# Kernel optimization log

Measured on AMD Instinct MI355X. Metric: run time of the kernel, lower is better.

Reference implementation:

```python
import jax, jax.numpy as jnp
import numpy as np

H = 64  # hidden_dim


def _lstm_layer(x, w_ih, w_hh, b_ih, b_hh):
    # x: [B,T,I]; w_ih: [4H,I]; w_hh: [4H,H]; gate order (PyTorch): i,f,g,o
    B = x.shape[0]
    xp = jnp.einsum('bti,gi->btg', x, w_ih) + b_ih + b_hh  # [B,T,4H]
    h0 = jnp.zeros((B, H), x.dtype)
    c0 = jnp.zeros((B, H), x.dtype)

    def step(carry, xt):
        h, c = carry
        g = xt + h @ w_hh.T  # [B,4H]
        i, f, gg, o = jnp.split(g, 4, axis=-1)
        c = jax.nn.sigmoid(f) * c + jax.nn.sigmoid(i) * jnp.tanh(gg)
        h = jax.nn.sigmoid(o) * jnp.tanh(c)
        return (h, c), h

    _, ys = jax.lax.scan(step, (h0, c0), xp.transpose(1, 0, 2))  # [T,B,H]
    return ys.transpose(1, 0, 2)


def _gru_layer(x, w_ih, w_hh, b_ih, b_hh):
    # x: [B,T,I]; w_ih: [3H,I]; w_hh: [3H,H]; gate order (PyTorch): r,z,n
    B = x.shape[0]
    xp = jnp.einsum('bti,gi->btg', x, w_ih) + b_ih  # [B,T,3H]
    h0 = jnp.zeros((B, H), x.dtype)

    def step(h, xt):
        hp = h @ w_hh.T + b_hh  # [B,3H]
        xr, xz, xn = jnp.split(xt, 3, axis=-1)
        hr, hz, hn = jnp.split(hp, 3, axis=-1)
        r = jax.nn.sigmoid(xr + hr)
        z = jax.nn.sigmoid(xz + hz)
        n = jnp.tanh(xn + r * hn)
        h = (1.0 - z) * n + z * h
        return h, h

    _, ys = jax.lax.scan(step, h0, xp.transpose(1, 0, 2))
    return ys.transpose(1, 0, 2)


def setup_inputs() -> dict:
    key = jax.random.key(0)
    ks = jax.random.split(key, 20)
    s = 1.0 / np.sqrt(H)  # PyTorch default uniform(-1/sqrt(H), 1/sqrt(H))
    u = lambda k, shp: jax.random.uniform(k, shp, jnp.float32, -s, s)
    B, T, I = 2048, 512, 1
    return {
        'x': jax.random.normal(ks[0], (B, T, I), jnp.float32),
        # LSTM layer 0 (input I) and layer 1 (input H)
        'lw_ih0': u(ks[1], (4 * H, I)), 'lw_hh0': u(ks[2], (4 * H, H)),
        'lb_ih0': u(ks[3], (4 * H,)), 'lb_hh0': u(ks[4], (4 * H,)),
        'lw_ih1': u(ks[5], (4 * H, H)), 'lw_hh1': u(ks[6], (4 * H, H)),
        'lb_ih1': u(ks[7], (4 * H,)), 'lb_hh1': u(ks[8], (4 * H,)),
        # GRU layer 0 and 1 (input H)
        'gw_ih0': u(ks[9], (3 * H, H)), 'gw_hh0': u(ks[10], (3 * H, H)),
        'gb_ih0': u(ks[11], (3 * H,)), 'gb_hh0': u(ks[12], (3 * H,)),
        'gw_ih1': u(ks[13], (3 * H, H)), 'gw_hh1': u(ks[14], (3 * H, H)),
        'gb_ih1': u(ks[15], (3 * H,)), 'gb_hh1': u(ks[16], (3 * H,)),
        # fc head
        'fc_w': u(ks[17], (1, H)), 'fc_b': u(ks[18], (1,)),
    }


def reference(x, lw_ih0, lw_hh0, lb_ih0, lb_hh0, lw_ih1, lw_hh1, lb_ih1, lb_hh1,
              gw_ih0, gw_hh0, gb_ih0, gb_hh0, gw_ih1, gw_hh1, gb_ih1, gb_hh1,
              fc_w, fc_b):
    out = _lstm_layer(x, lw_ih0, lw_hh0, lb_ih0, lb_hh0)
    out = _lstm_layer(out, lw_ih1, lw_hh1, lb_ih1, lb_hh1)
    out = _gru_layer(out, gw_ih0, gw_hh0, gb_ih0, gb_hh0)
    out = _gru_layer(out, gw_ih1, gw_hh1, gb_ih1, gb_hh1)
    return out[:, -1, :] @ fc_w.T + fc_b  # [B,1]
```

## Files before the change

### kernel.cpp

```cpp
#include <hip/hip_runtime.h>


#define TT 512
#define SR 72
#define SLOT (16 * SR)
#define LOG2E 1.44269504f

typedef __attribute__((ext_vector_type(8))) short bfrag;
typedef __attribute__((ext_vector_type(4))) float facc;

#define MFMA(a,b,c) __builtin_amdgcn_mfma_f32_16x16x32_bf16((a),(b),(c),0,0,0)

__device__ __forceinline__ float sigmP(float u){
  return __builtin_amdgcn_rcpf(1.0f + __builtin_amdgcn_exp2f(u));
}
__device__ __forceinline__ float tanhP(float u){
  return 2.0f * __builtin_amdgcn_rcpf(1.0f + __builtin_amdgcn_exp2f(u)) - 1.0f;
}
__device__ __forceinline__ void spin_ge(volatile int* p, int tgt){
  while (*p < tgt) {}
}
__device__ __forceinline__ facc bcast4(float v){
  facc b; b[0] = v; b[1] = v; b[2] = v; b[3] = v; return b;
}
__device__ __forceinline__ short f2bf(float f){
  union { float f; unsigned u; } v; v.f = f;
  return (short)((v.u + 0x7fffu + ((v.u >> 16) & 1u)) >> 16);
}
__device__ __forceinline__ unsigned pk_bf16(float lo, float hi){
  unsigned r;
  asm("v_cvt_pk_bf16_f32 %0, %1, %2" : "=v"(r) : "v"(lo), "v"(hi));
  return r;
}

__global__ __launch_bounds__(1024) void rnn_fused(
    const float* __restrict__ x,
    const float* __restrict__ lw_ih0, const float* __restrict__ lw_hh0,
    const float* __restrict__ lb_ih0, const float* __restrict__ lb_hh0,
    const float* __restrict__ lw_ih1, const float* __restrict__ lw_hh1,
    const float* __restrict__ lb_ih1, const float* __restrict__ lb_hh1,
    const float* __restrict__ gw_ih0, const float* __restrict__ gw_hh0,
    const float* __restrict__ gb_ih0, const float* __restrict__ gb_hh0,
    const float* __restrict__ gw_ih1, const float* __restrict__ gw_hh1,
    const float* __restrict__ gb_ih1, const float* __restrict__ gb_hh1,
    const float* __restrict__ fc_w, const float* __restrict__ fc_b,
    float* __restrict__ out)
{
  __shared__ __align__(16) short S0[4 * SLOT];
  __shared__ __align__(16) short S1[4 * SLOT];
  __shared__ __align__(16) short S2[4 * SLOT];
  __shared__ __align__(16) short S3[4 * SLOT];
  __shared__ float xs[8][TT];
  __shared__ float hfin[8][68];
  __shared__ int cnt[4];

  const int tid = threadIdx.x;
  const int w     = tid >> 6;
  const int layer = w >> 2;
  const int lo4   = w & 3;
  const int l   = tid & 63;
  const int lq  = l >> 4;
  const int lc  = l & 15;
  const int kb  = lq * 8;
  const int rb0 = blockIdx.x * 8;
  const int wrbase = (4 * lq) * SR + lo4 * 16 + lc;
  volatile int* vc = cnt;

  const float SS  = -LOG2E;
  const float ST2 = -2.0f * LOG2E;

  {
    const int idx = tid * 4;
    const int row = idx >> 9, t0 = idx & 511;
    *(float4*)&xs[row][t0] = *(const float4*)(x + (rb0 + row) * TT + t0);
  }
  for (int i = tid; i < 4 * SLOT; i += 1024) {
    S0[i] = 0; S1[i] = 0; S2[i] = 0; S3[i] = 0;
  }
  if (tid < 4) cnt[tid] = 0;
  __syncthreads();

  if (layer == 0) {
    bfrag wf[4][2];
    float wxs[4];
    facc b4[4];
    #pragma unroll
    for (int G = 0; G < 4; ++G) {
      const float sc = (G == 2) ? ST2 : SS;
      const int col = G * 64 + lo4 * 16 + lc;
      #pragma unroll
      for (int kt = 0; kt < 2; ++kt) {
        bfrag f;
        #pragma unroll
        for (int j = 0; j < 8; ++j)
          f[j] = f2bf(sc * lw_hh0[col * 64 + kt * 32 + kb + j]);
        wf[G][kt] = f;
      }
      wxs[G] = sc * lw_ih0[col];
      b4[G]  = bcast4(sc * (lb_ih0[col] + lb_hh0[col]));
    }
    float c0[2] = {0.f, 0.f};
    for (int tb = 0; tb < TT / 4; ++tb) {
      const float4 xv0 = *(const float4*)&xs[2 * lq][tb * 4];
      const float4 xv1 = *(const float4*)&xs[2 * lq + 1][tb * 4];
      const float* xp0 = (const float*)&xv0;
      const float* xp1 = (const float*)&xv1;
      #pragma unroll
      for (int u = 0; u < 4; ++u) {
        const int t = tb * 4 + u;
        if (tb >= 1) spin_ge(vc + 1, 4 * (t - 3));
        if (tb > 0 || u > 0) spin_ge(vc + 0, 4 * t);
        __threadfence_block();
        const short* s = S0 + ((u + 3) & 3) * SLOT;
        const bfrag a0 = *(const bfrag*)(s + lc * SR + kb);
        const bfrag a1 = *(const bfrag*)(s + lc * SR + 32 + kb);
        facc acc[4];
        #pragma unroll
        for (int G = 0; G < 4; ++G) {
          facc z = MFMA(a0, wf[G][0], b4[G]);
          z = MFMA(a1, wf[G][1], z);
          acc[G] = z;
        }
        float hh[2];
        #pragma unroll
        for (int m = 0; m < 2; ++m) {
          const float xv = m ? xp1[u] : xp0[u];
          const float i_ = sigmP(acc[0][m] + xv * wxs[0]);
          const float f_ = sigmP(acc[1][m] + xv * wxs[1]);
          const float g_ = tanhP(acc[2][m] + xv * wxs[2]);
          const float o_ = sigmP(acc[3][m] + xv * wxs[3]);
          c0[m] = f_ * c0[m] + i_ * g_;
          hh[m] = o_ * tanhP(c0[m] * ST2);
        }
        const unsigned pk = pk_bf16(hh[0], hh[1]);
        short* d = S0 + u * SLOT;
        d[wrbase]      = (short)pk;
        d[wrbase + SR] = (short)(pk >> 16);
        __threadfence_block();
        if (l == 0) atomicAdd(&cnt[0], 1);
      }
    }
  } else if (layer == 1) {
    bfrag wxf[4][2], whf[4][2];
    facc b4[4];
    #pragma unroll
    for (int G = 0; G < 4; ++G) {
      const float sc = (G == 2) ? ST2 : SS;
      const int col = G * 64 + lo4 * 16 + lc;
      #pragma unroll
      for (int kt = 0; kt < 2; ++kt) {
        bfrag f0, f1;
        #pragma unroll
        for (int j = 0; j < 8; ++j) {
          const int o = col * 64 + kt * 32 + kb + j;
          f0[j] = f2bf(sc * lw_ih1[o]);
          f1[j] = f2bf(sc * lw_hh1[o]);
        }
        wxf[G][kt] = f0; whf[G][kt] = f1;
      }
      b4[G] = bcast4(sc * (lb_ih1[col] + lb_hh1[col]));
    }
    float c1[2] = {0.f, 0.f};
    for (int tb = 0; tb < TT / 4; ++tb) {
      #pragma unroll
      for (int u = 0; u < 4; ++u) {
        const int t = tb * 4 + u;
        if (tb >= 1) spin_ge(vc + 2, 4 * (t - 3));
        spin_ge(vc + 0, 4 * (t + 1));
        if (tb > 0 || u > 0) spin_ge(vc + 1, 4 * t);
        __threadfence_block();
        const short* sx = S0 + u * SLOT;
        const short* sh = S1 + ((u + 3) & 3) * SLOT;
        const bfrag ax0 = *(const bfrag*)(sx + lc * SR + kb);
        const bfrag ax1 = *(const bfrag*)(sx + lc * SR + 32 + kb);
        const bfrag ah0 = *(const bfrag*)(sh + lc * SR + kb);
        const bfrag ah1 = *(const bfrag*)(sh + lc * SR + 32 + kb);
        facc acc[4];
        #pragma unroll
        for (int G = 0; G < 4; ++G) {
          facc z = MFMA(ax0, wxf[G][0], b4[G]);
          z = MFMA(ax1, wxf[G][1], z);
          z = MFMA(ah0, whf[G][0], z);
          z = MFMA(ah1, whf[G][1], z);
          acc[G] = z;
        }
        float hh[2];
        #pragma unroll
        for (int m = 0; m < 2; ++m) {
          const float i_ = sigmP(acc[0][m]);
          const float f_ = sigmP(acc[1][m]);
          const float g_ = tanhP(acc[2][m]);
          const float o_ = sigmP(acc[3][m]);
          c1[m] = f_ * c1[m] + i_ * g_;
          hh[m] = o_ * tanhP(c1[m] * ST2);
        }
        const unsigned pk = pk_bf16(hh[0], hh[1]);
        short* d = S1 + u * SLOT;
        d[wrbase]      = (short)pk;
        d[wrbase + SR] = (short)(pk >> 16);
        __threadfence_block();
        if (l == 0) atomicAdd(&cnt[1], 1);
      }
    }
  } else if (layer == 2) {
    bfrag gxf[3][2], ghf[3][2];
    facc brz4[2], bnx4, bnh4;
    #pragma unroll
    for (int G = 0; G < 3; ++G) {
      const float sc = (G == 2) ? ST2 : SS;
      const int col = G * 64 + lo4 * 16 + lc;
      #pragma unroll
      for (int kt = 0; kt < 2; ++kt) {
        bfrag f0, f1;
        #pragma unroll
        for (int j = 0; j < 8; ++j) {
          const int o = col * 64 + kt * 32 + kb + j;
          f0[j] = f2bf(sc * gw_ih0[o]);
          f1[j] = f2bf(sc * gw_hh0[o]);
        }
        gxf[G][kt] = f0; ghf[G][kt] = f1;
      }
      if (G < 2) brz4[G] = bcast4(sc * (gb_ih0[col] + gb_hh0[col]));
      else { bnx4 = bcast4(sc * gb_ih0[col]); bnh4 = bcast4(sc * gb_hh0[col]); }
    }
    float h2[2] = {0.f, 0.f};
    for (int tb = 0; tb < TT / 4; ++tb) {
      #pragma unroll
      for (int u = 0; u < 4; ++u) {
        const int t = tb * 4 + u;
        if (tb >= 1) spin_ge(vc + 3, 4 * (t - 3));
        spin_ge(vc + 1, 4 * (t + 1));
        if (tb > 0 || u > 0) spin_ge(vc + 2, 4 * t);
        __threadfence_block();
        const short* sx = S1 + u * SLOT;
        const short* sh = S2 + ((u + 3) & 3) * SLOT;
        const bfrag ax0 = *(const bfrag*)(sx + lc * SR + kb);
        const bfrag ax1 = *(const bfrag*)(sx + lc * SR + 32 + kb);
        const bfrag ah0 = *(const bfrag*)(sh + lc * SR + kb);
        const bfrag ah1 = *(const bfrag*)(sh + lc * SR + 32 + kb);
        facc rz[2], axn, ahn;
        #pragma unroll
        for (int G = 0; G < 2; ++G) {
          facc z = MFMA(ax0, gxf[G][0], brz4[G]);
          z = MFMA(ax1, gxf[G][1], z);
          z = MFMA(ah0, ghf[G][0], z);
          z = MFMA(ah1, ghf[G][1], z);
          rz[G] = z;
        }
        axn = MFMA(ax0, gxf[2][0], bnx4);
        axn = MFMA(ax1, gxf[2][1], axn);
        ahn = MFMA(ah0, ghf[2][0], bnh4);
        ahn = MFMA(ah1, ghf[2][1], ahn);
        float hh[2];
        #pragma unroll
        for (int m = 0; m < 2; ++m) {
          const float r_ = sigmP(rz[0][m]);
          const float z_ = sigmP(rz[1][m]);
          const float n_ = tanhP(axn[m] + r_ * ahn[m]);
          h2[m] = n_ + z_ * (h2[m] - n_);
          hh[m] = h2[m];
        }
        const unsigned pk = pk_bf16(hh[0], hh[1]);
        short* d = S2 + u * SLOT;
        d[wrbase]      = (short)pk;
        d[wrbase + SR] = (short)(pk >> 16);
        __threadfence_block();
        if (l == 0) atomicAdd(&cnt[2], 1);
      }
    }
  } else {
    bfrag gxf[3][2], ghf[3][2];
    facc brz4[2], bnx4, bnh4;
    #pragma unroll
    for (int G = 0; G < 3; ++G) {
      const float sc = (G == 2) ? ST2 : SS;
      const int col = G * 64 + lo4 * 16 + lc;
      #pragma unroll
      for (int kt = 0; kt < 2; ++kt) {
        bfrag f0, f1;
        #pragma unroll
        for (int j = 0; j < 8; ++j) {
          const int o = col * 64 + kt * 32 + kb + j;
          f0[j] = f2bf(sc * gw_ih1[o]);
          f1[j] = f2bf(sc * gw_hh1[o]);
        }
        gxf[G][kt] = f0; ghf[G][kt] = f1;
      }
      if (G < 2) brz4[G] = bcast4(sc * (gb_ih1[col] + gb_hh1[col]));
      else { bnx4 = bcast4(sc * gb_ih1[col]); bnh4 = bcast4(sc * gb_hh1[col]); }
    }
    float h3[2] = {0.f, 0.f};
    for (int tb = 0; tb < TT / 4; ++tb) {
      #pragma unroll
      for (int u = 0; u < 4; ++u) {
        const int t = tb * 4 + u;
        spin_ge(vc + 2, 4 * (t + 1));
        if (tb > 0 || u > 0) spin_ge(vc + 3, 4 * t);
        __threadfence_block();
        const short* sx = S2 + u * SLOT;
        const short* sh = S3 + ((u + 3) & 3) * SLOT;
        const bfrag ax0 = *(const bfrag*)(sx + lc * SR + kb);
        const bfrag ax1 = *(const bfrag*)(sx + lc * SR + 32 + kb);
        const bfrag ah0 = *(const bfrag*)(sh + lc * SR + kb);
        const bfrag ah1 = *(const bfrag*)(sh + lc * SR + 32 + kb);
        facc rz[2], axn, ahn;
        #pragma unroll
        for (int G = 0; G < 2; ++G) {
          facc z = MFMA(ax0, gxf[G][0], brz4[G]);
          z = MFMA(ax1, gxf[G][1], z);
          z = MFMA(ah0, ghf[G][0], z);
          z = MFMA(ah1, ghf[G][1], z);
          rz[G] = z;
        }
        axn = MFMA(ax0, gxf[2][0], bnx4);
        axn = MFMA(ax1, gxf[2][1], axn);
        ahn = MFMA(ah0, ghf[2][0], bnh4);
        ahn = MFMA(ah1, ghf[2][1], ahn);
        float hh[2];
        #pragma unroll
        for (int m = 0; m < 2; ++m) {
          const float r_ = sigmP(rz[0][m]);
          const float z_ = sigmP(rz[1][m]);
          const float n_ = tanhP(axn[m] + r_ * ahn[m]);
          h3[m] = n_ + z_ * (h3[m] - n_);
          hh[m] = h3[m];
        }
        const unsigned pk = pk_bf16(hh[0], hh[1]);
        short* d = S3 + u * SLOT;
        d[wrbase]      = (short)pk;
        d[wrbase + SR] = (short)(pk >> 16);
        __threadfence_block();
        if (l == 0) atomicAdd(&cnt[3], 1);
      }
    }
    #pragma unroll
    for (int m = 0; m < 2; ++m)
      hfin[2 * lq + m][lo4 * 16 + lc] = h3[m];
  }

  __syncthreads();
  if (tid < 8) {
    float s = fc_b[0];
    #pragma unroll 8
    for (int d = 0; d < 64; ++d) s += hfin[tid][d] * fc_w[d];
    out[rb0 + tid] = s;
  }
}

extern "C" void kernel_launch(void* const* d_in, const int* in_sizes, int n_in,
                              void* d_out, int out_size, void* d_ws, size_t ws_size,
                              hipStream_t stream) {
  const float* x      = (const float*)d_in[0];
  const float* lw_ih0 = (const float*)d_in[1];
  const float* lw_hh0 = (const float*)d_in[2];
  const float* lb_ih0 = (const float*)d_in[3];
  const float* lb_hh0 = (const float*)d_in[4];
  const float* lw_ih1 = (const float*)d_in[5];
  const float* lw_hh1 = (const float*)d_in[6];
  const float* lb_ih1 = (const float*)d_in[7];
  const float* lb_hh1 = (const float*)d_in[8];
  const float* gw_ih0 = (const float*)d_in[9];
  const float* gw_hh0 = (const float*)d_in[10];
  const float* gb_ih0 = (const float*)d_in[11];
  const float* gb_hh0 = (const float*)d_in[12];
  const float* gw_ih1 = (const float*)d_in[13];
  const float* gw_hh1 = (const float*)d_in[14];
  const float* gb_ih1 = (const float*)d_in[15];
  const float* gb_hh1 = (const float*)d_in[16];
  const float* fc_w   = (const float*)d_in[17];
  const float* fc_b   = (const float*)d_in[18];

  rnn_fused<<<dim3(2048 / 8), dim3(1024), 0, stream>>>(
      x, lw_ih0, lw_hh0, lb_ih0, lb_hh0, lw_ih1, lw_hh1, lb_ih1, lb_hh1,
      gw_ih0, gw_hh0, gb_ih0, gb_hh0, gw_ih1, gw_hh1, gb_ih1, gb_hh1,
      fc_w, fc_b, (float*)d_out);
}
```

Before: 400.5 us.

## Replace atomic counters with per-wave flags and hoist input-projection MFMAs before recurrent wait

Each layer's inter-wave synchronisation moves from one shared atomic counter per layer to four per-wave flag slots. Each wave writes its own slot with a plain store, and readers spin on the minimum of the four. In layers 1-3 the input-projection MFMAs now run as soon as the previous layer's output is ready, and the wait on the same layer's recurrent state happens only before the hidden-state MFMAs. This is meant to take atomic contention off the critical path and overlap input projection with waiting on the recurrence. The trailing __threadfence_block after each spin is dropped, which could weaken the ordering between the flag read and the LDS data reads.

```diff
diff --git a/kernel.cpp b/kernel.cpp
--- a/kernel.cpp
+++ b/kernel.cpp
@@ -17,8 +17,13 @@
 __device__ __forceinline__ float tanhP(float u){
   return 2.0f * __builtin_amdgcn_rcpf(1.0f + __builtin_amdgcn_exp2f(u)) - 1.0f;
 }
-__device__ __forceinline__ void spin_ge(volatile int* p, int tgt){
-  while (*p < tgt) {}
+__device__ __forceinline__ void spin_grp(volatile int* f, int tgt){
+  for (;;) {
+    const int a = f[0], b = f[1], c = f[2], d = f[3];
+    const int m0 = a < b ? a : b;
+    const int m1 = c < d ? c : d;
+    if ((m0 < m1 ? m0 : m1) >= tgt) return;
+  }
 }
 __device__ __forceinline__ facc bcast4(float v){
   facc b; b[0] = v; b[1] = v; b[2] = v; b[3] = v; return b;
@@ -52,7 +57,7 @@
   __shared__ __align__(16) short S3[4 * SLOT];
   __shared__ float xs[8][TT];
   __shared__ float hfin[8][68];
-  __shared__ int cnt[4];
+  __shared__ int flg[4][4];
 
   const int tid = threadIdx.x;
   const int w     = tid >> 6;
@@ -64,7 +69,10 @@
   const int kb  = lq * 8;
   const int rb0 = blockIdx.x * 8;
   const int wrbase = (4 * lq) * SR + lo4 * 16 + lc;
-  volatile int* vc = cnt;
+  volatile int* F0 = flg[0];
+  volatile int* F1 = flg[1];
+  volatile int* F2 = flg[2];
+  volatile int* F3 = flg[3];
 
   const float SS  = -LOG2E;
   const float ST2 = -2.0f * LOG2E;
@@ -77,7 +85,7 @@
   for (int i = tid; i < 4 * SLOT; i += 1024) {
     S0[i] = 0; S1[i] = 0; S2[i] = 0; S3[i] = 0;
   }
-  if (tid < 4) cnt[tid] = 0;
+  if (tid < 16) flg[tid >> 2][tid & 3] = 0;
   __syncthreads();
 
   if (layer == 0) {
@@ -108,9 +116,8 @@
       #pragma unroll
       for (int u = 0; u < 4; ++u) {
         const int t = tb * 4 + u;
-        if (tb >= 1) spin_ge(vc + 1, 4 * (t - 3));
-        if (tb > 0 || u > 0) spin_ge(vc + 0, 4 * t);
-        __threadfence_block();
+        if (tb >= 1) spin_grp(F1, t - 3);
+        if (tb > 0 || u > 0) spin_grp(F0, t);
         const short* s = S0 + ((u + 3) & 3) * SLOT;
         const bfrag a0 = *(const bfrag*)(s + lc * SR + kb);
         const bfrag a1 = *(const bfrag*)(s + lc * SR + 32 + kb);
@@ -137,7 +144,7 @@
         d[wrbase]      = (short)pk;
         d[wrbase + SR] = (short)(pk >> 16);
         __threadfence_block();
-        if (l == 0) atomicAdd(&cnt[0], 1);
+        if (l == 0) F0[lo4] = t + 1;
       }
     }
   } else if (layer == 1) {
@@ -165,24 +172,26 @@
       #pragma unroll
       for (int u = 0; u < 4; ++u) {
         const int t = tb * 4 + u;
-        if (tb >= 1) spin_ge(vc + 2, 4 * (t - 3));
-        spin_ge(vc + 0, 4 * (t + 1));
-        if (tb > 0 || u > 0) spin_ge(vc + 1, 4 * t);
-        __threadfence_block();
+        spin_grp(F0, t + 1);
         const short* sx = S0 + u * SLOT;
-        const short* sh = S1 + ((u + 3) & 3) * SLOT;
         const bfrag ax0 = *(const bfrag*)(sx + lc * SR + kb);
         const bfrag ax1 = *(const bfrag*)(sx + lc * SR + 32 + kb);
-        const bfrag ah0 = *(const bfrag*)(sh + lc * SR + kb);
-        const bfrag ah1 = *(const bfrag*)(sh + lc * SR + 32 + kb);
         facc acc[4];
         #pragma unroll
         for (int G = 0; G < 4; ++G) {
           facc z = MFMA(ax0, wxf[G][0], b4[G]);
           z = MFMA(ax1, wxf[G][1], z);
-          z = MFMA(ah0, whf[G][0], z);
-          z = MFMA(ah1, whf[G][1], z);
           acc[G] = z;
+        }
+        if (tb >= 1) spin_grp(F2, t - 3);
+        if (tb > 0 || u > 0) spin_grp(F1, t);
+        const short* sh = S1 + ((u + 3) & 3) * SLOT;
+        const bfrag ah0 = *(const bfrag*)(sh + lc * SR + kb);
+        const bfrag ah1 = *(const bfrag*)(sh + lc * SR + 32 + kb);
+        #pragma unroll
+        for (int G = 0; G < 4; ++G) {
+          acc[G] = MFMA(ah0, whf[G][0], acc[G]);
+          acc[G] = MFMA(ah1, whf[G][1], acc[G]);
         }
         float hh[2];
         #pragma unroll
@@ -199,7 +208,7 @@
         d[wrbase]      = (short)pk;
         d[wrbase + SR] = (short)(pk >> 16);
         __threadfence_block();
-        if (l == 0) atomicAdd(&cnt[1], 1);
+        if (l == 0) F1[lo4] = t + 1;
       }
     }
   } else if (layer == 2) {
@@ -228,29 +237,31 @@
       #pragma unroll
       for (int u = 0; u < 4; ++u) {
         const int t = tb * 4 + u;
-        if (tb >= 1) spin_ge(vc + 3, 4 * (t - 3));
-        spin_ge(vc + 1, 4 * (t + 1));
-        if (tb > 0 || u > 0) spin_ge(vc + 2, 4 * t);
-        __threadfence_block();
+        spin_grp(F1, t + 1);
         const short* sx = S1 + u * SLOT;
-        const short* sh = S2 + ((u + 3) & 3) * SLOT;
         const bfrag ax0 = *(const bfrag*)(sx + lc * SR + kb);
         const bfrag ax1 = *(const bfrag*)(sx + lc * SR + 32 + kb);
-        const bfrag ah0 = *(const bfrag*)(sh + lc * SR + kb);
-        const bfrag ah1 = *(const bfrag*)(sh + lc * SR + 32 + kb);
-        facc rz[2], axn, ahn;
+        facc rz[2], axn;
         #pragma unroll
         for (int G = 0; G < 2; ++G) {
           facc z = MFMA(ax0, gxf[G][0], brz4[G]);
           z = MFMA(ax1, gxf[G][1], z);
-          z = MFMA(ah0, ghf[G][0], z);
-          z = MFMA(ah1, ghf[G][1], z);
           rz[G] = z;
         }
         axn = MFMA(ax0, gxf[2][0], bnx4);
         axn = MFMA(ax1, gxf[2][1], axn);
-        ahn = MFMA(ah0, ghf[2][0], bnh4);
+        if (tb >= 1) spin_grp(F3, t - 3);
+        if (tb > 0 || u > 0) spin_grp(F2, t);
+        const short* sh = S2 + ((u + 3) & 3) * SLOT;
+        const bfrag ah0 = *(const bfrag*)(sh + lc * SR + kb);
+        const bfrag ah1 = *(const bfrag*)(sh + lc * SR + 32 + kb);
+        facc ahn = MFMA(ah0, ghf[2][0], bnh4);
         ahn = MFMA(ah1, ghf[2][1], ahn);
+        #pragma unroll
+        for (int G = 0; G < 2; ++G) {
+          rz[G] = MFMA(ah0, ghf[G][0], rz[G]);
+          rz[G] = MFMA(ah1, ghf[G][1], rz[G]);
+        }
         float hh[2];
         #pragma unroll
         for (int m = 0; m < 2; ++m) {
@@ -265,7 +276,7 @@
         d[wrbase]      = (short)pk;
         d[wrbase + SR] = (short)(pk >> 16);
         __threadfence_block();
-        if (l == 0) atomicAdd(&cnt[2], 1);
+        if (l == 0) F2[lo4] = t + 1;
       }
     }
   } else {
@@ -294,28 +305,30 @@
       #pragma unroll
       for (int u = 0; u < 4; ++u) {
         const int t = tb * 4 + u;
-        spin_ge(vc + 2, 4 * (t + 1));
-        if (tb > 0 || u > 0) spin_ge(vc + 3, 4 * t);
-        __threadfence_block();
+        spin_grp(F2, t + 1);
         const short* sx = S2 + u * SLOT;
-        const short* sh = S3 + ((u + 3) & 3) * SLOT;
         const bfrag ax0 = *(const bfrag*)(sx + lc * SR + kb);
         const bfrag ax1 = *(const bfrag*)(sx + lc * SR + 32 + kb);
-        const bfrag ah0 = *(const bfrag*)(sh + lc * SR + kb);
-        const bfrag ah1 = *(const bfrag*)(sh + lc * SR + 32 + kb);
-        facc rz[2], axn, ahn;
+        facc rz[2], axn;
         #pragma unroll
         for (int G = 0; G < 2; ++G) {
           facc z = MFMA(ax0, gxf[G][0], brz4[G]);
           z = MFMA(ax1, gxf[G][1], z);
-          z = MFMA(ah0, ghf[G][0], z);
-          z = MFMA(ah1, ghf[G][1], z);
           rz[G] = z;
         }
         axn = MFMA(ax0, gxf[2][0], bnx4);
         axn = MFMA(ax1, gxf[2][1], axn);
-        ahn = MFMA(ah0, ghf[2][0], bnh4);
+        if (tb > 0 || u > 0) spin_grp(F3, t);
+        const short* sh = S3 + ((u + 3) & 3) * SLOT;
+        const bfrag ah0 = *(const bfrag*)(sh + lc * SR + kb);
+        const bfrag ah1 = *(const bfrag*)(sh + lc * SR + 32 + kb);
+        facc ahn = MFMA(ah0, ghf[2][0], bnh4);
         ahn = MFMA(ah1, ghf[2][1], ahn);
+        #pragma unroll
+        for (int G = 0; G < 2; ++G) {
+          rz[G] = MFMA(ah0, ghf[G][0], rz[G]);
+          rz[G] = MFMA(ah1, ghf[G][1], rz[G]);
+        }
         float hh[2];
         #pragma unroll
         for (int m = 0; m < 2; ++m) {
@@ -330,7 +343,7 @@
         d[wrbase]      = (short)pk;
         d[wrbase + SR] = (short)(pk >> 16);
         __threadfence_block();
-        if (l == 0) atomicAdd(&cnt[3], 1);
+        if (l == 0) F3[lo4] = t + 1;
       }
     }
     #pragma unroll
```

Measured after the change: 541.9 us. +35.3%, slower.
